# Optimization experiments

Hardware: AMD Instinct MI355X
Metric: run time of the kernel (lower is better)

The kernel has to match this reference:

```python
import jax, jax.numpy as jnp
import numpy as np

NUM_TOKENS = 8192
HIDDEN = 4096
NUM_EXPERTS = 8
EXPERT_INTER = 2048  # intermediate_size // num_experts // tp_size (tp=1)
VOCAB = 32000


def setup_inputs() -> dict:
    key = jax.random.key(0)
    k1, k2, k3, k4 = jax.random.split(key, 4)
    x = jax.random.normal(k1, (NUM_TOKENS, HIDDEN), dtype=jnp.float32)
    token_ids = jax.random.randint(k2, (NUM_TOKENS,), 0, VOCAB, dtype=jnp.int64)
    # kaiming-uniform-like init scale ~ 1/sqrt(fan_in)
    gate_up_proj = jax.random.normal(k3, (NUM_EXPERTS, HIDDEN, 2 * EXPERT_INTER), dtype=jnp.float32) * (1.0 / np.sqrt(HIDDEN))
    down_proj = jax.random.normal(k4, (NUM_EXPERTS, EXPERT_INTER, HIDDEN), dtype=jnp.float32) * (1.0 / np.sqrt(EXPERT_INTER))
    return {"x": x, "token_ids": token_ids, "gate_up_proj": gate_up_proj, "down_proj": down_proj}


def reference(x, token_ids, gate_up_proj, down_proj):
    num_experts = gate_up_proj.shape[0]
    expert_inter = down_proj.shape[1]
    # route: expert_id = clamp(token_id, 0, vocab-1) % num_experts
    expert_ids = jnp.clip(token_ids, 0, VOCAB - 1) % num_experts
    out = jnp.zeros_like(x)
    # fixed small loop over experts (structurally distinct weights);
    # mask tokens instead of dynamic-size slicing (jit-safe, same math).
    for eid in range(num_experts):
        mask = (expert_ids == eid)[:, None].astype(x.dtype)  # [N,1]
        xe = x * mask                                        # zero out other experts' tokens
        gu = xe @ gate_up_proj[eid]                          # [N, 2*inter]
        gate = gu[:, :expert_inter]
        up = gu[:, expert_inter:]
        inter = jax.nn.silu(gate) * up                       # SwiGLU
        out = out + (inter @ down_proj[eid]) * mask
    return out
```

## Files before the change

### kernel.cpp

```cpp
#include <hip/hip_runtime.h>
#include <hip/hip_bf16.h>

#define TOKENS 8192
#define HID 4096
#define NEXP 8
#define INTER 2048
#define VOCABM1 31999
#define MAXROWS 9216
#define MAXTILES 72

typedef float f32x4 __attribute__((ext_vector_type(4)));
typedef __bf16 bf16x8 __attribute__((ext_vector_type(8)));
typedef short sh4 __attribute__((ext_vector_type(4)));

#define WS_NTILES  0
#define WS_TEXP    64
#define WS_TROW    512
#define WS_TNV     1024
#define WS_PERM    4096
#define WS_ROWTOK  40960
#define WS_XS      131072
#define WS_INTER   (WS_XS + (size_t)MAXROWS * HID * 2)
#define WS_NEED    (WS_INTER + (size_t)MAXROWS * INTER * 2)

__device__ __forceinline__ int iclamp(int v, int lo, int hi) {
    return v < lo ? lo : (v > hi ? hi : v);
}
__device__ __forceinline__ unsigned short f2b(float f) {
    __hip_bfloat16 h = __float2bfloat16(f);
    unsigned short u; __builtin_memcpy(&u, &h, 2); return u;
}
__device__ __forceinline__ unsigned pk2(float a, float b) {
    return (unsigned)f2b(a) | ((unsigned)f2b(b) << 16);
}
__device__ __forceinline__ void gld16(const void* g, void* l) {
    __builtin_amdgcn_global_load_lds((const __attribute__((address_space(1))) void*)g,
                                     (__attribute__((address_space(3))) void*)l,
                                     16, 0, 0);
}
__device__ __forceinline__ bf16x8 ldfrag(const unsigned short* p) {
    sh4 lo = *(const sh4*)p;
    sh4 hi = *(const sh4*)(p + 4);
    struct { sh4 a, b; } s{lo, hi};
    return __builtin_bit_cast(bf16x8, s);
}

__global__ void route_kernel(const int* __restrict__ ids, char* __restrict__ ws) {
    __shared__ int cnt[NEXP], base[NEXP], cur[NEXP];
    int tid = threadIdx.x;
    if (tid < NEXP) { cnt[tid] = 0; cur[tid] = 0; }
    __syncthreads();
    for (int i = tid; i < TOKENS; i += blockDim.x) {
        int v = iclamp(ids[i], 0, VOCABM1);
        atomicAdd(&cnt[v & 7], 1);
    }
    __syncthreads();
    if (tid == 0) {
        int* texp = (int*)(ws + WS_TEXP);
        int* trow = (int*)(ws + WS_TROW);
        int* tnv  = (int*)(ws + WS_TNV);
        int pb = 0, ntl = 0;
        for (int e = 0; e < NEXP; e++) {
            base[e] = pb;
            int ne = cnt[e];
            int t = (ne + 127) >> 7;
            for (int j = 0; j < t; j++) {
                texp[ntl] = e;
                trow[ntl] = pb + j * 128;
                int rem = ne - j * 128;
                tnv[ntl] = rem < 128 ? rem : 128;
                ntl++;
            }
            pb += t * 128;
        }
        *(int*)(ws + WS_NTILES) = ntl;
    }
    __syncthreads();
    int* perm = (int*)(ws + WS_PERM);
    int* rt   = (int*)(ws + WS_ROWTOK);
    for (int i = tid; i < TOKENS; i += blockDim.x) {
        int v = iclamp(ids[i], 0, VOCABM1);
        int e = v & 7;
        int p = atomicAdd(&cur[e], 1);
        int slot = base[e] + p;
        perm[i] = slot;
        rt[slot] = i;
    }
}

__global__ void gather_cast(const float* __restrict__ x, char* __restrict__ ws) {
    const int* perm = (const int*)(ws + WS_PERM);
    unsigned short* xs = (unsigned short*)(ws + WS_XS);
    int tok = blockIdx.x;
    int slot = perm[tok];
    const float4* src = (const float4*)(x + (size_t)tok * HID);
    uint2* dst = (uint2*)(xs + (size_t)slot * HID);
    for (int j = threadIdx.x; j < HID / 4; j += blockDim.x) {
        float4 f = src[j];
        dst[j] = make_uint2(pk2(f.x, f.y), pk2(f.z, f.w));
    }
}

__global__ __launch_bounds__(256, 2)
void gemm1_kernel(char* __restrict__ ws, const float* __restrict__ gup) {
    int nt = *(const int*)(ws + WS_NTILES);
    int by = blockIdx.y;
    if (by >= nt) return;
    int e    = ((const int*)(ws + WS_TEXP))[by];
    int row0 = ((const int*)(ws + WS_TROW))[by];
    int nv   = ((const int*)(ws + WS_TNV))[by];

    const unsigned short* xs = (const unsigned short*)(ws + WS_XS);
    unsigned short* ib = (unsigned short*)(ws + WS_INTER);

    __shared__ __align__(16) unsigned short sA[128 * 32];
    __shared__ __align__(16) unsigned short sBg[128 * 36];
    __shared__ __align__(16) unsigned short sBu[128 * 36];

    int tid = threadIdx.x, w = tid >> 6, l = tid & 63;
    int wm = w & 1, wn = w >> 1, m = l & 15, q = l >> 4;

    const unsigned short* Ab = xs + (size_t)row0 * HID;
    const float* Wg = gup + (size_t)e * HID * (2 * INTER) + (size_t)blockIdx.x * 128;
    const float* Wu = Wg + INTER;

    int c0 = tid, c1 = 256 + tid;
    int ar0 = c0 >> 2, ak0 = (c0 & 3) * 8;
    int ar1 = c1 >> 2, ak1 = (c1 & 3) * 8;
    unsigned short* aD0 = sA + (w * 64) * 8;
    unsigned short* aD1 = sA + (256 + w * 64) * 8;

    int n = tid & 127, kh = (tid >> 7) * 16;

    f32x4 accg[4][4], accu[4][4];
#pragma unroll
    for (int i = 0; i < 4; i++)
#pragma unroll
        for (int j = 0; j < 4; j++) { accg[i][j] = (f32x4)0.0f; accu[i][j] = (f32x4)0.0f; }

    for (int k0 = 0; k0 < HID; k0 += 32) {
        gld16(Ab + (size_t)ar0 * HID + k0 + ak0, aD0);
        gld16(Ab + (size_t)ar1 * HID + k0 + ak1, aD1);
#pragma unroll
        for (int g = 0; g < 4; g++) {
            int kb = kh + g * 4;
            const float* wp = Wg + (size_t)(k0 + kb) * (2 * INTER) + n;
            *(uint2*)(sBg + n * 36 + kb) =
                make_uint2(pk2(wp[0], wp[2 * INTER]), pk2(wp[4 * INTER], wp[6 * INTER]));
            const float* vp = Wu + (size_t)(k0 + kb) * (2 * INTER) + n;
            *(uint2*)(sBu + n * 36 + kb) =
                make_uint2(pk2(vp[0], vp[2 * INTER]), pk2(vp[4 * INTER], vp[6 * INTER]));
        }
        __syncthreads();

        bf16x8 af[4], bg[4], bu[4];
#pragma unroll
        for (int mi = 0; mi < 4; mi++)
            af[mi] = *(const bf16x8*)(sA + ((wm * 64 + mi * 16 + m) * 32 + q * 8));
#pragma unroll
        for (int ni = 0; ni < 4; ni++) {
            int nb = (wn * 64 + ni * 16 + m) * 36 + q * 8;
            bg[ni] = ldfrag(sBg + nb);
            bu[ni] = ldfrag(sBu + nb);
        }
#pragma unroll
        for (int mi = 0; mi < 4; mi++)
#pragma unroll
            for (int ni = 0; ni < 4; ni++) {
                accg[mi][ni] = __builtin_amdgcn_mfma_f32_16x16x32_bf16(af[mi], bg[ni], accg[mi][ni], 0, 0, 0);
                accu[mi][ni] = __builtin_amdgcn_mfma_f32_16x16x32_bf16(af[mi], bu[ni], accu[mi][ni], 0, 0, 0);
            }
        __syncthreads();
    }

#pragma unroll
    for (int mi = 0; mi < 4; mi++)
#pragma unroll
        for (int r = 0; r < 4; r++) {
            int rl = wm * 64 + mi * 16 + q * 4 + r;
            if (rl < nv) {
                size_t o = (size_t)(row0 + rl) * INTER + blockIdx.x * 128 + wn * 64 + m;
#pragma unroll
                for (int ni = 0; ni < 4; ni++) {
                    float g = accg[mi][ni][r];
                    float u = accu[mi][ni][r];
                    float s = g / (1.0f + __expf(-g));
                    ib[o + ni * 16] = f2b(s * u);
                }
            }
        }
}

__global__ __launch_bounds__(256, 2)
void gemm2_kernel(char* __restrict__ ws, const float* __restrict__ dwn, float* __restrict__ out) {
    int nt = *(const int*)(ws + WS_NTILES);
    int by = blockIdx.y;
    if (by >= nt) return;
    int e    = ((const int*)(ws + WS_TEXP))[by];
    int row0 = ((const int*)(ws + WS_TROW))[by];
    int nv   = ((const int*)(ws + WS_TNV))[by];
    const int* rowtok = (const int*)(ws + WS_ROWTOK);
    const unsigned short* ib = (const unsigned short*)(ws + WS_INTER);

    __shared__ __align__(16) unsigned short sA[128 * 32];
    __shared__ __align__(16) unsigned short sB[128 * 36];

    int tid = threadIdx.x, w = tid >> 6, l = tid & 63;
    int wm = w & 1, wn = w >> 1, m = l & 15, q = l >> 4;

    const unsigned short* Ab = ib + (size_t)row0 * INTER;
    const float* W = dwn + (size_t)e * INTER * HID + (size_t)blockIdx.x * 128;

    int c0 = tid, c1 = 256 + tid;
    int ar0 = c0 >> 2, ak0 = (c0 & 3) * 8;
    int ar1 = c1 >> 2, ak1 = (c1 & 3) * 8;
    unsigned short* aD0 = sA + (w * 64) * 8;
    unsigned short* aD1 = sA + (256 + w * 64) * 8;

    int n = tid & 127, kh = (tid >> 7) * 16;

    f32x4 acc[4][4];
#pragma unroll
    for (int i = 0; i < 4; i++)
#pragma unroll
        for (int j = 0; j < 4; j++) acc[i][j] = (f32x4)0.0f;

    for (int k0 = 0; k0 < INTER; k0 += 32) {
        gld16(Ab + (size_t)ar0 * INTER + k0 + ak0, aD0);
        gld16(Ab + (size_t)ar1 * INTER + k0 + ak1, aD1);
#pragma unroll
        for (int g = 0; g < 4; g++) {
            int kb = kh + g * 4;
            const float* wp = W + (size_t)(k0 + kb) * HID + n;
            *(uint2*)(sB + n * 36 + kb) =
                make_uint2(pk2(wp[0], wp[HID]), pk2(wp[2 * HID], wp[3 * HID]));
        }
        __syncthreads();

        bf16x8 af[4], bfr[4];
#pragma unroll
        for (int mi = 0; mi < 4; mi++)
            af[mi] = *(const bf16x8*)(sA + ((wm * 64 + mi * 16 + m) * 32 + q * 8));
#pragma unroll
        for (int ni = 0; ni < 4; ni++)
            bfr[ni] = ldfrag(sB + (wn * 64 + ni * 16 + m) * 36 + q * 8);
#pragma unroll
        for (int mi = 0; mi < 4; mi++)
#pragma unroll
            for (int ni = 0; ni < 4; ni++)
                acc[mi][ni] = __builtin_amdgcn_mfma_f32_16x16x32_bf16(af[mi], bfr[ni], acc[mi][ni], 0, 0, 0);
        __syncthreads();
    }

#pragma unroll
    for (int mi = 0; mi < 4; mi++)
#pragma unroll
        for (int r = 0; r < 4; r++) {
            int rl = wm * 64 + mi * 16 + q * 4 + r;
            if (rl < nv) {
                int tok = rowtok[row0 + rl];
                size_t o = (size_t)tok * HID + blockIdx.x * 128 + wn * 64 + m;
#pragma unroll
                for (int ni = 0; ni < 4; ni++) out[o + ni * 16] = acc[mi][ni][r];
            }
        }
}

extern "C" void kernel_launch(void* const* d_in, const int* in_sizes, int n_in,
                              void* d_out, int out_size, void* d_ws, size_t ws_size,
                              hipStream_t stream) {
    const float* x   = (const float*)d_in[0];
    const int*   ids = (const int*)d_in[1];
    const float* gup = (const float*)d_in[2];
    const float* dwn = (const float*)d_in[3];
    char* ws = (char*)d_ws;
    if (ws_size < WS_NEED) return;

    hipLaunchKernelGGL(route_kernel, dim3(1), dim3(1024), 0, stream, ids, ws);
    hipLaunchKernelGGL(gather_cast, dim3(TOKENS), dim3(256), 0, stream, x, ws);
    hipLaunchKernelGGL(gemm1_kernel, dim3(16, MAXTILES), dim3(256), 0, stream, ws, gup);
    hipLaunchKernelGGL(gemm2_kernel, dim3(32, MAXTILES), dim3(256), 0, stream, ws, dwn, (float*)d_out);
}
```

Measured before the change: 1.697 ms.

## Pre-transpose and cast expert weights to bf16 before MoE GEMMs

Adds a transpose-and-cast kernel that converts the gate_up and down weights from fp32 into K-contiguous bf16 copies in the workspace. New GEMM kernels then load both operands straight into LDS with direct global-to-LDS loads, replacing the old in-loop fp32 weight conversion. The extra pass reads all weights once in fp32 and writes them as bf16 each call, and it needs a large workspace. If the workspace is too small, the code falls back to the old fp32-weight kernels.

Result: faster. 1.626 ms (-4.2%).

```diff
diff --git a/kernel.cpp b/kernel.cpp
--- a/kernel.cpp
+++ b/kernel.cpp
@@ -21,7 +21,10 @@
 #define WS_ROWTOK  40960
 #define WS_XS      131072
 #define WS_INTER   (WS_XS + (size_t)MAXROWS * HID * 2)
-#define WS_NEED    (WS_INTER + (size_t)MAXROWS * INTER * 2)
+#define WS_GUPT    (WS_INTER + (size_t)MAXROWS * INTER * 2)
+#define WS_DWNT    WS_GUPT
+#define WS_NEED_BIG (WS_GUPT + (size_t)NEXP * (2 * INTER) * HID * 2)
+#define WS_NEED_SMALL WS_GUPT
 
 __device__ __forceinline__ int iclamp(int v, int lo, int hi) {
     return v < lo ? lo : (v > hi ? hi : v);
@@ -101,8 +104,189 @@
     }
 }
 
+__global__ __launch_bounds__(256)
+void convT_kernel(const float* __restrict__ src, unsigned short* __restrict__ dst,
+                  int R, int C) {
+    __shared__ float tile[64][65];
+    int e = blockIdx.z;
+    const float* S = src + (size_t)e * R * C;
+    unsigned short* D = dst + (size_t)e * C * R;
+    int r0 = blockIdx.y * 64, c0 = blockIdx.x * 64;
+    int t = threadIdx.x;
+    int lr = t >> 4;
+    int lc = (t & 15) * 4;
+#pragma unroll
+    for (int i = 0; i < 4; i++) {
+        int rr = lr + i * 16;
+        float4 v = *(const float4*)(S + (size_t)(r0 + rr) * C + c0 + lc);
+        tile[rr][lc + 0] = v.x; tile[rr][lc + 1] = v.y;
+        tile[rr][lc + 2] = v.z; tile[rr][lc + 3] = v.w;
+    }
+    __syncthreads();
+#pragma unroll
+    for (int i = 0; i < 2; i++) {
+        int g = t + i * 256;
+        int n = g >> 3;
+        int kg = (g & 7) * 8;
+        uint4 o;
+        o.x = pk2(tile[kg + 0][n], tile[kg + 1][n]);
+        o.y = pk2(tile[kg + 2][n], tile[kg + 3][n]);
+        o.z = pk2(tile[kg + 4][n], tile[kg + 5][n]);
+        o.w = pk2(tile[kg + 6][n], tile[kg + 7][n]);
+        *(uint4*)(D + (size_t)(c0 + n) * R + r0 + kg) = o;
+    }
+}
+
 __global__ __launch_bounds__(256, 2)
-void gemm1_kernel(char* __restrict__ ws, const float* __restrict__ gup) {
+void gemm1_bf(char* __restrict__ ws) {
+    int nt = *(const int*)(ws + WS_NTILES);
+    int by = blockIdx.y;
+    if (by >= nt) return;
+    int e    = ((const int*)(ws + WS_TEXP))[by];
+    int row0 = ((const int*)(ws + WS_TROW))[by];
+    int nv   = ((const int*)(ws + WS_TNV))[by];
+
+    const unsigned short* xs   = (const unsigned short*)(ws + WS_XS);
+    const unsigned short* gupT = (const unsigned short*)(ws + WS_GUPT);
+    unsigned short* ib = (unsigned short*)(ws + WS_INTER);
+
+    __shared__ __align__(16) unsigned short sA [128 * 32];
+    __shared__ __align__(16) unsigned short sBg[128 * 32];
+    __shared__ __align__(16) unsigned short sBu[128 * 32];
+
+    int tid = threadIdx.x, w = tid >> 6, l = tid & 63;
+    int wm = w & 1, wn = w >> 1, m = l & 15, q = l >> 4;
+
+    const unsigned short* Ab = xs + (size_t)row0 * HID;
+    const unsigned short* Bg = gupT + ((size_t)e * (2 * INTER) + blockIdx.x * 128) * HID;
+    const unsigned short* Bu = Bg + (size_t)INTER * HID;
+
+    size_t a0 = (size_t)(tid >> 2) * HID + (tid & 3) * 8;
+    size_t a1 = a0 + (size_t)64 * HID;
+    int d0 = w * 512, d1 = 2048 + w * 512;
+
+    f32x4 accg[4][4], accu[4][4];
+#pragma unroll
+    for (int i = 0; i < 4; i++)
+#pragma unroll
+        for (int j = 0; j < 4; j++) { accg[i][j] = (f32x4)0.0f; accu[i][j] = (f32x4)0.0f; }
+
+    for (int k0 = 0; k0 < HID; k0 += 32) {
+        gld16(Ab + a0 + k0, sA + d0);
+        gld16(Ab + a1 + k0, sA + d1);
+        gld16(Bg + a0 + k0, sBg + d0);
+        gld16(Bg + a1 + k0, sBg + d1);
+        gld16(Bu + a0 + k0, sBu + d0);
+        gld16(Bu + a1 + k0, sBu + d1);
+        __syncthreads();
+
+        bf16x8 af[4], bg[4], bu[4];
+#pragma unroll
+        for (int mi = 0; mi < 4; mi++)
+            af[mi] = *(const bf16x8*)(sA + (wm * 64 + mi * 16 + m) * 32 + q * 8);
+#pragma unroll
+        for (int ni = 0; ni < 4; ni++) {
+            int nb = (wn * 64 + ni * 16 + m) * 32 + q * 8;
+            bg[ni] = *(const bf16x8*)(sBg + nb);
+            bu[ni] = *(const bf16x8*)(sBu + nb);
+        }
+#pragma unroll
+        for (int mi = 0; mi < 4; mi++)
+#pragma unroll
+            for (int ni = 0; ni < 4; ni++) {
+                accg[mi][ni] = __builtin_amdgcn_mfma_f32_16x16x32_bf16(af[mi], bg[ni], accg[mi][ni], 0, 0, 0);
+                accu[mi][ni] = __builtin_amdgcn_mfma_f32_16x16x32_bf16(af[mi], bu[ni], accu[mi][ni], 0, 0, 0);
+            }
+        __syncthreads();
+    }
+
+#pragma unroll
+    for (int mi = 0; mi < 4; mi++)
+#pragma unroll
+        for (int r = 0; r < 4; r++) {
+            int rl = wm * 64 + mi * 16 + q * 4 + r;
+            if (rl < nv) {
+                size_t o = (size_t)(row0 + rl) * INTER + blockIdx.x * 128 + wn * 64 + m;
+#pragma unroll
+                for (int ni = 0; ni < 4; ni++) {
+                    float g = accg[mi][ni][r];
+                    float u = accu[mi][ni][r];
+                    float s = g / (1.0f + __expf(-g));
+                    ib[o + ni * 16] = f2b(s * u);
+                }
+            }
+        }
+}
+
+__global__ __launch_bounds__(256, 2)
+void gemm2_bf(char* __restrict__ ws, float* __restrict__ out) {
+    int nt = *(const int*)(ws + WS_NTILES);
+    int by = blockIdx.y;
+    if (by >= nt) return;
+    int e    = ((const int*)(ws + WS_TEXP))[by];
+    int row0 = ((const int*)(ws + WS_TROW))[by];
+    int nv   = ((const int*)(ws + WS_TNV))[by];
+    const int* rowtok = (const int*)(ws + WS_ROWTOK);
+    const unsigned short* ib   = (const unsigned short*)(ws + WS_INTER);
+    const unsigned short* dwnT = (const unsigned short*)(ws + WS_DWNT);
+
+    __shared__ __align__(16) unsigned short sA[128 * 32];
+    __shared__ __align__(16) unsigned short sB[128 * 32];
+
+    int tid = threadIdx.x, w = tid >> 6, l = tid & 63;
+    int wm = w & 1, wn = w >> 1, m = l & 15, q = l >> 4;
+
+    const unsigned short* Ab = ib + (size_t)row0 * INTER;
+    const unsigned short* Bb = dwnT + ((size_t)e * HID + blockIdx.x * 128) * INTER;
+
+    size_t a0 = (size_t)(tid >> 2) * INTER + (tid & 3) * 8;
+    size_t a1 = a0 + (size_t)64 * INTER;
+    int d0 = w * 512, d1 = 2048 + w * 512;
+
+    f32x4 acc[4][4];
+#pragma unroll
+    for (int i = 0; i < 4; i++)
+#pragma unroll
+        for (int j = 0; j < 4; j++) acc[i][j] = (f32x4)0.0f;
+
+    for (int k0 = 0; k0 < INTER; k0 += 32) {
+        gld16(Ab + a0 + k0, sA + d0);
+        gld16(Ab + a1 + k0, sA + d1);
+        gld16(Bb + a0 + k0, sB + d0);
+        gld16(Bb + a1 + k0, sB + d1);
+        __syncthreads();
+
+        bf16x8 af[4], bfr[4];
+#pragma unroll
+        for (int mi = 0; mi < 4; mi++)
+            af[mi] = *(const bf16x8*)(sA + (wm * 64 + mi * 16 + m) * 32 + q * 8);
+#pragma unroll
+        for (int ni = 0; ni < 4; ni++)
+            bfr[ni] = *(const bf16x8*)(sB + (wn * 64 + ni * 16 + m) * 32 + q * 8);
+#pragma unroll
+        for (int mi = 0; mi < 4; mi++)
+#pragma unroll
+            for (int ni = 0; ni < 4; ni++)
+                acc[mi][ni] = __builtin_amdgcn_mfma_f32_16x16x32_bf16(af[mi], bfr[ni], acc[mi][ni], 0, 0, 0);
+        __syncthreads();
+    }
+
+#pragma unroll
+    for (int mi = 0; mi < 4; mi++)
+#pragma unroll
+        for (int r = 0; r < 4; r++) {
+            int rl = wm * 64 + mi * 16 + q * 4 + r;
+            if (rl < nv) {
+                int tok = rowtok[row0 + rl];
+                size_t o = (size_t)tok * HID + blockIdx.x * 128 + wn * 64 + m;
+#pragma unroll
+                for (int ni = 0; ni < 4; ni++) out[o + ni * 16] = acc[mi][ni][r];
+            }
+        }
+}
+
+__global__ __launch_bounds__(256, 2)
+void gemm1_f32(char* __restrict__ ws, const float* __restrict__ gup) {
     int nt = *(const int*)(ws + WS_NTILES);
     int by = blockIdx.y;
     if (by >= nt) return;
@@ -192,7 +376,7 @@
 }
 
 __global__ __launch_bounds__(256, 2)
-void gemm2_kernel(char* __restrict__ ws, const float* __restrict__ dwn, float* __restrict__ out) {
+void gemm2_f32(char* __restrict__ ws, const float* __restrict__ dwn, float* __restrict__ out) {
     int nt = *(const int*)(ws + WS_NTILES);
     int by = blockIdx.y;
     if (by >= nt) return;
@@ -274,10 +458,20 @@
     const float* gup = (const float*)d_in[2];
     const float* dwn = (const float*)d_in[3];
     char* ws = (char*)d_ws;
-    if (ws_size < WS_NEED) return;
-
-    hipLaunchKernelGGL(route_kernel, dim3(1), dim3(1024), 0, stream, ids, ws);
-    hipLaunchKernelGGL(gather_cast, dim3(TOKENS), dim3(256), 0, stream, x, ws);
-    hipLaunchKernelGGL(gemm1_kernel, dim3(16, MAXTILES), dim3(256), 0, stream, ws, gup);
-    hipLaunchKernelGGL(gemm2_kernel, dim3(32, MAXTILES), dim3(256), 0, stream, ws, dwn, (float*)d_out);
-}
+
+    if (ws_size >= WS_NEED_BIG) {
+        hipLaunchKernelGGL(route_kernel, dim3(1), dim3(1024), 0, stream, ids, ws);
+        hipLaunchKernelGGL(gather_cast, dim3(TOKENS), dim3(256), 0, stream, x, ws);
+        hipLaunchKernelGGL(convT_kernel, dim3((2 * INTER) / 64, HID / 64, NEXP), dim3(256), 0, stream,
+                           gup, (unsigned short*)(ws + WS_GUPT), HID, 2 * INTER);
+        hipLaunchKernelGGL(gemm1_bf, dim3(16, MAXTILES), dim3(256), 0, stream, ws);
+        hipLaunchKernelGGL(convT_kernel, dim3(HID / 64, INTER / 64, NEXP), dim3(256), 0, stream,
+                           dwn, (unsigned short*)(ws + WS_DWNT), INTER, HID);
+        hipLaunchKernelGGL(gemm2_bf, dim3(32, MAXTILES), dim3(256), 0, stream, ws, (float*)d_out);
+    } else if (ws_size >= WS_NEED_SMALL) {
+        hipLaunchKernelGGL(route_kernel, dim3(1), dim3(1024), 0, stream, ids, ws);
+        hipLaunchKernelGGL(gather_cast, dim3(TOKENS), dim3(256), 0, stream, x, ws);
+        hipLaunchKernelGGL(gemm1_f32, dim3(16, MAXTILES), dim3(256), 0, stream, ws, gup);
+        hipLaunchKernelGGL(gemm2_f32, dim3(32, MAXTILES), dim3(256), 0, stream, ws, dwn, (float*)d_out);
+    }
+}
```
